# Kernel optimization log

Hardware: AMD Instinct MI355X
Metric: run time of the kernel (lower is better)

Reference implementation:

```python
import jax, jax.numpy as jnp
import numpy as np

EPS = 1e-5  # torch BatchNorm1d default
N_BLOCKS = 15


def setup_inputs() -> dict:
    key = jax.random.key(0)
    ks = jax.random.split(key, 5)
    B = 131072
    x = jax.random.normal(ks[0], (B, 29), dtype=jnp.float32)
    # first block params (Linear(29,59) + BN(59))
    W0 = jax.random.normal(ks[1], (59, 29), dtype=jnp.float32) * (1.0 / np.sqrt(29))
    b0 = jnp.zeros((59,), dtype=jnp.float32)
    g0 = jnp.ones((59,), dtype=jnp.float32)
    bt0 = jnp.zeros((59,), dtype=jnp.float32)
    # remaining 14 blocks (Linear(59,59) + BN(59)), stacked
    Ws = jax.random.normal(ks[2], (14, 59, 59), dtype=jnp.float32) * (1.0 / np.sqrt(59))
    bs = jnp.zeros((14, 59), dtype=jnp.float32)
    gs = jnp.ones((14, 59), dtype=jnp.float32)
    bts = jnp.zeros((14, 59), dtype=jnp.float32)
    return {"x": x, "W0": W0, "b0": b0, "g0": g0, "bt0": bt0,
            "Ws": Ws, "bs": bs, "gs": gs, "bts": bts}


def _block(x, W, b, g, bt):
    # Linear -> ReLU -> BatchNorm1d (training mode: batch stats, biased var)
    h = jnp.maximum(x @ W.T + b, 0.0)          # [B, 59]
    mu = jnp.mean(h, axis=0)                    # [59]
    var = jnp.mean((h - mu) ** 2, axis=0)       # biased variance
    return (h - mu) * jax.lax.rsqrt(var + EPS) * g + bt


def reference(x, W0, b0, g0, bt0, Ws, bs, gs, bts):
    h = _block(x, W0, b0, g0, bt0)

    def step(carry, p):
        W, b, g, bt = p
        return _block(carry, W, b, g, bt), None

    h, _ = jax.lax.scan(step, h, (Ws, bs, gs, bts))
    return h
```

## Files before the change

### kernel.cpp

```cpp
#include <hip/hip_runtime.h>

#define NTHR  256
#define F     59
#define K0    29
#define NB    15
#define B     131072
#define RPB   64
#define NBLK  (B / RPB)
#define NSLC  32
#define FPW   16
#define HSTR  68
#define YSTR  68

#define ACC_PER_LAYER (F * NSLC * 2)
#define ACC_TOTAL     (NB * ACC_PER_LAYER)
#define WT_OFF_B      ((size_t)ACC_TOTAL * 8)
#define WT_FLOATS     ((K0 + 14 * F) * 64)
#define HB_OFF_B      (WT_OFF_B + (size_t)WT_FLOATS * 4)

__global__ void transpose_w(const float* __restrict__ W0,
                            const float* __restrict__ Ws,
                            float* __restrict__ Wt)
{
  const int b = blockIdx.x;
  const float* W = (b == 0) ? W0 : Ws + (size_t)(b - 1) * F * F;
  const int K   = (b == 0) ? K0 : F;
  float* dst = (b == 0) ? Wt : Wt + (size_t)K0 * 64 + (size_t)(b - 1) * F * 64;
  for (int i = threadIdx.x; i < K * 64; i += blockDim.x) {
    int k = i >> 6, j = i & 63;
    dst[i] = (j < F) ? W[j * K + k] : 0.f;
  }
}

__device__ __forceinline__ void scsh_wave0(const double* __restrict__ acc_prev,
                                           const float* __restrict__ g,
                                           const float* __restrict__ bt,
                                           float2* scsh, int lane)
{
  if (lane < F) {
    const double* p = acc_prev + (size_t)lane * (NSLC * 2);
    double s1 = 0.0, s2 = 0.0;
    #pragma unroll
    for (int s = 0; s < NSLC; ++s) { s1 += p[2 * s]; s2 += p[2 * s + 1]; }
    const double inv = 1.0 / (double)B;
    double mu   = s1 * inv;
    double var  = fma(s2, inv, -mu * mu);
    double rstd = 1.0 / sqrt(var + 1e-5);
    double sc   = rstd * (double)g[lane];
    scsh[lane] = make_float2((float)sc, (float)fma(-mu, sc, (double)bt[lane]));
  }
}

template<int K, bool FIRST>
__global__ void __launch_bounds__(NTHR, 8)
layer_kernel(const float* __restrict__ in, const float* __restrict__ Wt,
             const float* __restrict__ bvec,
             const double* __restrict__ acc_prev,
             const float* __restrict__ g_prev, const float* __restrict__ bt_prev,
             float* __restrict__ hout, double* acc)
{
  __shared__ float lds[4 * FPW * YSTR];
  __shared__ __attribute__((aligned(16))) float2 scsh[64];

  const int tid   = threadIdx.x;
  const int lane  = tid & 63;
  const int qu    = __builtin_amdgcn_readfirstlane(tid >> 6);
  const int rowbase = blockIdx.x * RPB;
  const int slice   = blockIdx.x & (NSLC - 1);

  if (FIRST) {
    const float* xblk = in + (size_t)rowbase * K;
    for (int i = tid; i < RPB * K; i += NTHR) {
      int r = i / K, k = i - r * K;
      lds[r * 33 + k] = xblk[i];
    }
  } else {
    if (qu == 0) {
      scsh_wave0(acc_prev, g_prev, bt_prev, scsh, lane);
    } else {
      for (int i = tid - 64; i < K * 16; i += (NTHR - 64)) {
        int k = i >> 4, r4 = i & 15;
        float4 v = *(const float4*)(in + (size_t)k * B + rowbase + r4 * 4);
        *(float4*)&lds[k * HSTR + r4 * 4] = v;
      }
    }
  }
  __syncthreads();

  const int fbase = qu * FPW;
  float a0,a1,a2,a3,a4,a5,a6,a7,a8,a9,a10,a11,a12,a13,a14,a15;
  {
    #define BV(j) bvec[(fbase + j) > (F - 1) ? (F - 1) : (fbase + j)]
    a0=BV(0); a1=BV(1); a2=BV(2); a3=BV(3); a4=BV(4); a5=BV(5); a6=BV(6); a7=BV(7);
    a8=BV(8); a9=BV(9); a10=BV(10); a11=BV(11); a12=BV(12); a13=BV(13); a14=BV(14); a15=BV(15);
    #undef BV
  }

  #define FMA16(hk, wk)                                                     \
    a0  = fmaf(hk, (wk)[0],  a0);  a1  = fmaf(hk, (wk)[1],  a1);            \
    a2  = fmaf(hk, (wk)[2],  a2);  a3  = fmaf(hk, (wk)[3],  a3);            \
    a4  = fmaf(hk, (wk)[4],  a4);  a5  = fmaf(hk, (wk)[5],  a5);            \
    a6  = fmaf(hk, (wk)[6],  a6);  a7  = fmaf(hk, (wk)[7],  a7);            \
    a8  = fmaf(hk, (wk)[8],  a8);  a9  = fmaf(hk, (wk)[9],  a9);            \
    a10 = fmaf(hk, (wk)[10], a10); a11 = fmaf(hk, (wk)[11], a11);           \
    a12 = fmaf(hk, (wk)[12], a12); a13 = fmaf(hk, (wk)[13], a13);           \
    a14 = fmaf(hk, (wk)[14], a14); a15 = fmaf(hk, (wk)[15], a15);

  int k = 0;
  #pragma unroll 2
  for (; k + 2 <= K; k += 2) {
    float hk0, hk1;
    if (FIRST) {
      hk0 = lds[lane * 33 + k];
      hk1 = lds[lane * 33 + k + 1];
    } else {
      float4 s = *(const float4*)&scsh[k];
      hk0 = fmaf(lds[k * HSTR + lane],       s.x, s.y);
      hk1 = fmaf(lds[(k + 1) * HSTR + lane], s.z, s.w);
    }
    const float* wk0 = Wt + (size_t)k * 64 + fbase;
    const float* wk1 = wk0 + 64;
    FMA16(hk0, wk0)
    FMA16(hk1, wk1)
  }
  {
    float hk;
    if (FIRST) {
      hk = lds[lane * 33 + k];
    } else {
      float2 s = scsh[k];
      hk = fmaf(lds[k * HSTR + lane], s.x, s.y);
    }
    const float* wk = Wt + (size_t)k * 64 + fbase;
    FMA16(hk, wk)
  }
  #undef FMA16

  a0=fmaxf(a0,0.f); a1=fmaxf(a1,0.f); a2=fmaxf(a2,0.f); a3=fmaxf(a3,0.f);
  a4=fmaxf(a4,0.f); a5=fmaxf(a5,0.f); a6=fmaxf(a6,0.f); a7=fmaxf(a7,0.f);
  a8=fmaxf(a8,0.f); a9=fmaxf(a9,0.f); a10=fmaxf(a10,0.f); a11=fmaxf(a11,0.f);
  a12=fmaxf(a12,0.f); a13=fmaxf(a13,0.f); a14=fmaxf(a14,0.f); a15=fmaxf(a15,0.f);

  float* op = hout + rowbase + lane;
  #define ST(j, aj) if (fbase + j < F) op[(size_t)(fbase + j) * B] = aj;
  ST(0,a0)  ST(1,a1)  ST(2,a2)  ST(3,a3)  ST(4,a4)  ST(5,a5)  ST(6,a6)  ST(7,a7)
  ST(8,a8)  ST(9,a9)  ST(10,a10) ST(11,a11) ST(12,a12) ST(13,a13) ST(14,a14) ST(15,a15)
  #undef ST

  __syncthreads();

  float* ytq = lds + qu * (FPW * YSTR);
  ytq[0*YSTR+lane]=a0;   ytq[1*YSTR+lane]=a1;   ytq[2*YSTR+lane]=a2;
  ytq[3*YSTR+lane]=a3;   ytq[4*YSTR+lane]=a4;   ytq[5*YSTR+lane]=a5;
  ytq[6*YSTR+lane]=a6;   ytq[7*YSTR+lane]=a7;   ytq[8*YSTR+lane]=a8;
  ytq[9*YSTR+lane]=a9;   ytq[10*YSTR+lane]=a10; ytq[11*YSTR+lane]=a11;
  ytq[12*YSTR+lane]=a12; ytq[13*YSTR+lane]=a13; ytq[14*YSTR+lane]=a14;
  ytq[15*YSTR+lane]=a15;

  const int fl = lane >> 2, c = lane & 3;
  const float* yp = ytq + fl * YSTR + c * 16;
  float4 v0 = *(const float4*)(yp);
  float4 v1 = *(const float4*)(yp + 4);
  float4 v2 = *(const float4*)(yp + 8);
  float4 v3 = *(const float4*)(yp + 12);
  float s1 = ((v0.x+v0.y)+(v0.z+v0.w)) + ((v1.x+v1.y)+(v1.z+v1.w))
           + ((v2.x+v2.y)+(v2.z+v2.w)) + ((v3.x+v3.y)+(v3.z+v3.w));
  float s2 = 0.f;
  s2 = fmaf(v0.x,v0.x,s2); s2 = fmaf(v0.y,v0.y,s2); s2 = fmaf(v0.z,v0.z,s2); s2 = fmaf(v0.w,v0.w,s2);
  s2 = fmaf(v1.x,v1.x,s2); s2 = fmaf(v1.y,v1.y,s2); s2 = fmaf(v1.z,v1.z,s2); s2 = fmaf(v1.w,v1.w,s2);
  s2 = fmaf(v2.x,v2.x,s2); s2 = fmaf(v2.y,v2.y,s2); s2 = fmaf(v2.z,v2.z,s2); s2 = fmaf(v2.w,v2.w,s2);
  s2 = fmaf(v3.x,v3.x,s2); s2 = fmaf(v3.y,v3.y,s2); s2 = fmaf(v3.z,v3.z,s2); s2 = fmaf(v3.w,v3.w,s2);

  s1 += __shfl_xor(s1, 1, 64);  s2 += __shfl_xor(s2, 1, 64);
  s1 += __shfl_xor(s1, 2, 64);  s2 += __shfl_xor(s2, 2, 64);

  if (c == 0 && fbase + fl < F) {
    double* slot = acc + ((size_t)(fbase + fl) * NSLC + slice) * 2;
    atomicAdd(slot,     (double)s1);
    atomicAdd(slot + 1, (double)s2);
  }
}

__global__ void __launch_bounds__(NTHR, 8)
final_tr_kernel(const float* __restrict__ hT, const double* __restrict__ acc_last,
                const float* __restrict__ g, const float* __restrict__ bt,
                float* __restrict__ out)
{
  __shared__ float2 scsh[64];
  __shared__ float  ybuf[F * 64];
  const int tid  = threadIdx.x;
  const int lane = tid & 63;
  const int qu   = __builtin_amdgcn_readfirstlane(tid >> 6);
  const int rowbase = blockIdx.x * RPB;

  if (qu == 0) {
    scsh_wave0(acc_last, g, bt, scsh, lane);
  } else {
    for (int i = tid - 64; i < F * 16; i += (NTHR - 64)) {
      int j = i >> 4, r4 = i & 15;
      float4 v = *(const float4*)(hT + (size_t)j * B + rowbase + r4 * 4);
      *(float4*)&ybuf[j * 64 + r4 * 4] = v;
    }
  }
  __syncthreads();

  float* oblk = out + (size_t)rowbase * F;
  for (int i = tid; i < RPB * F; i += NTHR) {
    int r = i / F, j = i - r * F;
    float2 s = scsh[j];
    oblk[i] = fmaf(ybuf[j * 64 + r], s.x, s.y);
  }
}

extern "C" void kernel_launch(void* const* d_in, const int* in_sizes, int n_in,
                              void* d_out, int out_size, void* d_ws, size_t ws_size,
                              hipStream_t stream)
{
  const float* x   = (const float*)d_in[0];
  const float* W0  = (const float*)d_in[1];
  const float* b0  = (const float*)d_in[2];
  const float* g0  = (const float*)d_in[3];
  const float* bt0 = (const float*)d_in[4];
  const float* Ws  = (const float*)d_in[5];
  const float* bs  = (const float*)d_in[6];
  const float* gs  = (const float*)d_in[7];
  const float* bts = (const float*)d_in[8];
  float* out = (float*)d_out;

  double* acc = (double*)d_ws;
  float*  Wt  = (float*)((char*)d_ws + WT_OFF_B);
  float*  hB  = (float*)((char*)d_ws + HB_OFF_B);
  float*  hA  = out;

  hipMemsetAsync(d_ws, 0, (size_t)ACC_TOTAL * sizeof(double), stream);

  transpose_w<<<NB, NTHR, 0, stream>>>(W0, Ws, Wt);

  layer_kernel<K0, true><<<NBLK, NTHR, 0, stream>>>(
      x, Wt, b0, nullptr, nullptr, nullptr, hB, acc);

  for (int b = 1; b < NB; ++b) {
    const float* gp  = (b == 1) ? g0  : gs  + (size_t)(b - 2) * F;
    const float* btp = (b == 1) ? bt0 : bts + (size_t)(b - 2) * F;
    const float* src = (b & 1) ? hB : hA;
    float*       dst = (b & 1) ? hA : hB;
    const float* Wtb = Wt + (size_t)K0 * 64 + (size_t)(b - 1) * F * 64;
    layer_kernel<F, false><<<NBLK, NTHR, 0, stream>>>(
        src, Wtb, bs + (size_t)(b - 1) * F,
        acc + (size_t)(b - 1) * ACC_PER_LAYER, gp, btp,
        dst, acc + (size_t)b * ACC_PER_LAYER);
  }

  final_tr_kernel<<<NBLK, NTHR, 0, stream>>>(
      hB, acc + (size_t)(NB - 1) * ACC_PER_LAYER,
      gs + (size_t)(NB - 2) * F, bts + (size_t)(NB - 2) * F, out);
}
```

Baseline: 464.4 us.

## Fold BatchNorm scale/shift into next layer weights and bias via tiny fuse kernel

Adds a single-block fuse_w kernel before each hidden layer that computes BN statistics once and folds the scale into the transposed weights and the shift into the bias. Each layer kernel then no longer recomputes scale/shift per block or applies a per-element FMA to its inputs. The input tile is now stored row-major in LDS so the inner loop reads float4 chunks of K padded to 60/32. The cost is 14 extra small serial launches on the critical path and scattered scalar LDS stores during the transpose.

```diff
diff --git a/kernel.cpp b/kernel.cpp
--- a/kernel.cpp
+++ b/kernel.cpp
@@ -11,25 +11,70 @@
 #define FPW   16
 #define HSTR  68
 #define YSTR  68
+#define KC0   32
+#define KCN   60
 
 #define ACC_PER_LAYER (F * NSLC * 2)
 #define ACC_TOTAL     (NB * ACC_PER_LAYER)
 #define WT_OFF_B      ((size_t)ACC_TOTAL * 8)
-#define WT_FLOATS     ((K0 + 14 * F) * 64)
-#define HB_OFF_B      (WT_OFF_B + (size_t)WT_FLOATS * 4)
-
-__global__ void transpose_w(const float* __restrict__ W0,
+#define WT0_FLOATS    (KC0 * 64)
+#define WTN_FLOATS    (KCN * 64)
+#define WT_FLOATS     (WT0_FLOATS + 14 * WTN_FLOATS)
+#define BP_OFF_B      (WT_OFF_B + (size_t)WT_FLOATS * 4)
+#define HB_OFF_B      (BP_OFF_B + (size_t)NB * 64 * 4)
+
+__global__ void transpose_w(const float* __restrict__ W0, const float* __restrict__ b0,
                             const float* __restrict__ Ws,
-                            float* __restrict__ Wt)
+                            float* __restrict__ Wt, float* __restrict__ bp0)
 {
   const int b = blockIdx.x;
-  const float* W = (b == 0) ? W0 : Ws + (size_t)(b - 1) * F * F;
-  const int K   = (b == 0) ? K0 : F;
-  float* dst = (b == 0) ? Wt : Wt + (size_t)K0 * 64 + (size_t)(b - 1) * F * 64;
-  for (int i = threadIdx.x; i < K * 64; i += blockDim.x) {
-    int k = i >> 6, j = i & 63;
-    dst[i] = (j < F) ? W[j * K + k] : 0.f;
-  }
+  if (b == 0) {
+    for (int i = threadIdx.x; i < KC0 * 64; i += blockDim.x) {
+      int k = i >> 6, j = i & 63;
+      Wt[i] = (k < K0 && j < F) ? W0[j * K0 + k] : 0.f;
+    }
+    if (threadIdx.x < 64) bp0[threadIdx.x] = (threadIdx.x < F) ? b0[threadIdx.x] : 0.f;
+  } else {
+    float* dst = Wt + WT0_FLOATS + (size_t)(b - 1) * WTN_FLOATS;
+    const float* W = Ws + (size_t)(b - 1) * F * F;
+    for (int i = threadIdx.x; i < KCN * 64; i += blockDim.x) {
+      int k = i >> 6, j = i & 63;
+      dst[i] = (k < F && j < F) ? W[j * F + k] : 0.f;
+    }
+  }
+}
+
+__global__ void fuse_w(const double* __restrict__ acc_prev,
+                       const float* __restrict__ g, const float* __restrict__ bt,
+                       const float* __restrict__ bias,
+                       float* Wp, float* __restrict__ bp)
+{
+  __shared__ float  scf[64];
+  __shared__ double shd[64];
+  const int j = threadIdx.x;
+
+  if (j < F) {
+    const double* p = acc_prev + (size_t)j * (NSLC * 2);
+    double s1 = 0.0, s2 = 0.0;
+    #pragma unroll
+    for (int s = 0; s < NSLC; ++s) { s1 += p[2 * s]; s2 += p[2 * s + 1]; }
+    const double inv = 1.0 / (double)B;
+    double mu   = s1 * inv;
+    double var  = fma(s2, inv, -mu * mu);
+    double rstd = 1.0 / sqrt(var + 1e-5);
+    double sc   = rstd * (double)g[j];
+    scf[j] = (float)sc;
+    shd[j] = fma(-mu, sc, (double)bt[j]);
+  } else { scf[j] = 0.f; shd[j] = 0.0; }
+  __syncthreads();
+
+  double bacc = (j < F) ? (double)bias[j] : 0.0;
+  for (int k = 0; k < F; ++k) {
+    float w = Wp[k * 64 + j];
+    bacc = fma((double)w, shd[k], bacc);
+    Wp[k * 64 + j] = w * scf[k];
+  }
+  bp[j] = (float)bacc;
 }
 
 __device__ __forceinline__ void scsh_wave0(const double* __restrict__ acc_prev,
@@ -51,16 +96,13 @@
   }
 }
 
-template<int K, bool FIRST>
+template<int KC, bool FIRST>
 __global__ void __launch_bounds__(NTHR, 8)
-layer_kernel(const float* __restrict__ in, const float* __restrict__ Wt,
-             const float* __restrict__ bvec,
-             const double* __restrict__ acc_prev,
-             const float* __restrict__ g_prev, const float* __restrict__ bt_prev,
+layer_kernel(const float* __restrict__ in, const float* __restrict__ Wp,
+             const float* __restrict__ bp,
              float* __restrict__ hout, double* acc)
 {
-  __shared__ float lds[4 * FPW * YSTR];
-  __shared__ __attribute__((aligned(16))) float2 scsh[64];
+  __shared__ __attribute__((aligned(16))) float lds[4 * FPW * YSTR];
 
   const int tid   = threadIdx.x;
   const int lane  = tid & 63;
@@ -69,32 +111,27 @@
   const int slice   = blockIdx.x & (NSLC - 1);
 
   if (FIRST) {
-    const float* xblk = in + (size_t)rowbase * K;
-    for (int i = tid; i < RPB * K; i += NTHR) {
-      int r = i / K, k = i - r * K;
-      lds[r * 33 + k] = xblk[i];
+    for (int i = tid; i < RPB * KC0; i += NTHR) {
+      int r = i >> 5, k = i & 31;
+      lds[r * HSTR + k] = (k < K0) ? in[(size_t)(rowbase + r) * K0 + k] : 0.f;
     }
   } else {
-    if (qu == 0) {
-      scsh_wave0(acc_prev, g_prev, bt_prev, scsh, lane);
-    } else {
-      for (int i = tid - 64; i < K * 16; i += (NTHR - 64)) {
-        int k = i >> 4, r4 = i & 15;
-        float4 v = *(const float4*)(in + (size_t)k * B + rowbase + r4 * 4);
-        *(float4*)&lds[k * HSTR + r4 * 4] = v;
-      }
+    for (int i = tid; i < KCN * 16; i += NTHR) {
+      int k = i >> 4, r4 = i & 15;
+      float4 v = make_float4(0.f, 0.f, 0.f, 0.f);
+      if (k < F) v = *(const float4*)(in + (size_t)k * B + rowbase + r4 * 4);
+      lds[(4 * r4 + 0) * HSTR + k] = v.x;
+      lds[(4 * r4 + 1) * HSTR + k] = v.y;
+      lds[(4 * r4 + 2) * HSTR + k] = v.z;
+      lds[(4 * r4 + 3) * HSTR + k] = v.w;
     }
   }
   __syncthreads();
 
   const int fbase = qu * FPW;
-  float a0,a1,a2,a3,a4,a5,a6,a7,a8,a9,a10,a11,a12,a13,a14,a15;
-  {
-    #define BV(j) bvec[(fbase + j) > (F - 1) ? (F - 1) : (fbase + j)]
-    a0=BV(0); a1=BV(1); a2=BV(2); a3=BV(3); a4=BV(4); a5=BV(5); a6=BV(6); a7=BV(7);
-    a8=BV(8); a9=BV(9); a10=BV(10); a11=BV(11); a12=BV(12); a13=BV(13); a14=BV(14); a15=BV(15);
-    #undef BV
-  }
+  const float* bq = bp + fbase;
+  float a0=bq[0],a1=bq[1],a2=bq[2],a3=bq[3],a4=bq[4],a5=bq[5],a6=bq[6],a7=bq[7],
+        a8=bq[8],a9=bq[9],a10=bq[10],a11=bq[11],a12=bq[12],a13=bq[13],a14=bq[14],a15=bq[15];
 
   #define FMA16(hk, wk)                                                     \
     a0  = fmaf(hk, (wk)[0],  a0);  a1  = fmaf(hk, (wk)[1],  a1);            \
@@ -106,33 +143,15 @@
     a12 = fmaf(hk, (wk)[12], a12); a13 = fmaf(hk, (wk)[13], a13);           \
     a14 = fmaf(hk, (wk)[14], a14); a15 = fmaf(hk, (wk)[15], a15);
 
-  int k = 0;
-  #pragma unroll 2
-  for (; k + 2 <= K; k += 2) {
-    float hk0, hk1;
-    if (FIRST) {
-      hk0 = lds[lane * 33 + k];
-      hk1 = lds[lane * 33 + k + 1];
-    } else {
-      float4 s = *(const float4*)&scsh[k];
-      hk0 = fmaf(lds[k * HSTR + lane],       s.x, s.y);
-      hk1 = fmaf(lds[(k + 1) * HSTR + lane], s.z, s.w);
-    }
-    const float* wk0 = Wt + (size_t)k * 64 + fbase;
-    const float* wk1 = wk0 + 64;
-    FMA16(hk0, wk0)
-    FMA16(hk1, wk1)
-  }
-  {
-    float hk;
-    if (FIRST) {
-      hk = lds[lane * 33 + k];
-    } else {
-      float2 s = scsh[k];
-      hk = fmaf(lds[k * HSTR + lane], s.x, s.y);
-    }
-    const float* wk = Wt + (size_t)k * 64 + fbase;
-    FMA16(hk, wk)
+  const float* hrow = lds + lane * HSTR;
+  #pragma unroll 3
+  for (int c = 0; c < KC / 4; ++c) {
+    float4 hv = *(const float4*)(hrow + 4 * c);
+    const float* wk = Wp + (size_t)(4 * c) * 64 + fbase;
+    FMA16(hv.x, wk)
+    FMA16(hv.y, wk + 64)
+    FMA16(hv.z, wk + 128)
+    FMA16(hv.w, wk + 192)
   }
   #undef FMA16
 
@@ -166,10 +185,10 @@
   float s1 = ((v0.x+v0.y)+(v0.z+v0.w)) + ((v1.x+v1.y)+(v1.z+v1.w))
            + ((v2.x+v2.y)+(v2.z+v2.w)) + ((v3.x+v3.y)+(v3.z+v3.w));
   float s2 = 0.f;
-  s2 = fmaf(v0.x,v0.x,s2); s2 = fmaf(v0.y,v0.y,s2); s2 = fmaf(v0.z,v0.z,s2); s2 = fmaf(v0.w,v0.w,s2);
-  s2 = fmaf(v1.x,v1.x,s2); s2 = fmaf(v1.y,v1.y,s2); s2 = fmaf(v1.z,v1.z,s2); s2 = fmaf(v1.w,v1.w,s2);
-  s2 = fmaf(v2.x,v2.x,s2); s2 = fmaf(v2.y,v2.y,s2); s2 = fmaf(v2.z,v2.z,s2); s2 = fmaf(v2.w,v2.w,s2);
-  s2 = fmaf(v3.x,v3.x,s2); s2 = fmaf(v3.y,v3.y,s2); s2 = fmaf(v3.z,v3.z,s2); s2 = fmaf(v3.w,v3.w,s2);
+  s2=fmaf(v0.x,v0.x,s2); s2=fmaf(v0.y,v0.y,s2); s2=fmaf(v0.z,v0.z,s2); s2=fmaf(v0.w,v0.w,s2);
+  s2=fmaf(v1.x,v1.x,s2); s2=fmaf(v1.y,v1.y,s2); s2=fmaf(v1.z,v1.z,s2); s2=fmaf(v1.w,v1.w,s2);
+  s2=fmaf(v2.x,v2.x,s2); s2=fmaf(v2.y,v2.y,s2); s2=fmaf(v2.z,v2.z,s2); s2=fmaf(v2.w,v2.w,s2);
+  s2=fmaf(v3.x,v3.x,s2); s2=fmaf(v3.y,v3.y,s2); s2=fmaf(v3.z,v3.z,s2); s2=fmaf(v3.w,v3.w,s2);
 
   s1 += __shfl_xor(s1, 1, 64);  s2 += __shfl_xor(s2, 1, 64);
   s1 += __shfl_xor(s1, 2, 64);  s2 += __shfl_xor(s2, 2, 64);
@@ -229,26 +248,27 @@
 
   double* acc = (double*)d_ws;
   float*  Wt  = (float*)((char*)d_ws + WT_OFF_B);
+  float*  bp  = (float*)((char*)d_ws + BP_OFF_B);
   float*  hB  = (float*)((char*)d_ws + HB_OFF_B);
   float*  hA  = out;
 
   hipMemsetAsync(d_ws, 0, (size_t)ACC_TOTAL * sizeof(double), stream);
 
-  transpose_w<<<NB, NTHR, 0, stream>>>(W0, Ws, Wt);
-
-  layer_kernel<K0, true><<<NBLK, NTHR, 0, stream>>>(
-      x, Wt, b0, nullptr, nullptr, nullptr, hB, acc);
+  transpose_w<<<NB, NTHR, 0, stream>>>(W0, b0, Ws, Wt, bp);
+
+  layer_kernel<KC0, true><<<NBLK, NTHR, 0, stream>>>(x, Wt, bp, hB, acc);
 
   for (int b = 1; b < NB; ++b) {
     const float* gp  = (b == 1) ? g0  : gs  + (size_t)(b - 2) * F;
     const float* btp = (b == 1) ? bt0 : bts + (size_t)(b - 2) * F;
+    float* Wpb = Wt + WT0_FLOATS + (size_t)(b - 1) * WTN_FLOATS;
+    fuse_w<<<1, 64, 0, stream>>>(acc + (size_t)(b - 1) * ACC_PER_LAYER,
+                                 gp, btp, bs + (size_t)(b - 1) * F,
+                                 Wpb, bp + (size_t)b * 64);
     const float* src = (b & 1) ? hB : hA;
     float*       dst = (b & 1) ? hA : hB;
-    const float* Wtb = Wt + (size_t)K0 * 64 + (size_t)(b - 1) * F * 64;
-    layer_kernel<F, false><<<NBLK, NTHR, 0, stream>>>(
-        src, Wtb, bs + (size_t)(b - 1) * F,
-        acc + (size_t)(b - 1) * ACC_PER_LAYER, gp, btp,
-        dst, acc + (size_t)b * ACC_PER_LAYER);
+    layer_kernel<KCN, false><<<NBLK, NTHR, 0, stream>>>(
+        src, Wpb, bp + (size_t)b * 64, dst, acc + (size_t)b * ACC_PER_LAYER);
   }
 
   final_tr_kernel<<<NBLK, NTHR, 0, stream>>>(
```

Measured after the change: 463.1 us. About the same (-0.3%).
